# Kernel optimization log

Hardware: AMD Instinct MI355X
Metric: run time of the kernel (lower is better)

## Reference

```python
import jax, jax.numpy as jnp
import numpy as np
import math

EMBED_DIM = 1024
NUM_HEADS = 16
HEAD_DIM = EMBED_DIM // NUM_HEADS
B, S = 2, 2048


def setup_inputs() -> dict:
    key = jax.random.key(0)
    ks = jax.random.split(key, 13)
    sc = 1.0 / math.sqrt(EMBED_DIM)
    inp = {
        "query": jax.random.normal(ks[0], (B, S, EMBED_DIM), jnp.float32),
        "key": jax.random.normal(ks[1], (B, S, EMBED_DIM), jnp.float32),
        "value": jax.random.normal(ks[2], (B, S, EMBED_DIM), jnp.float32),
        "input_patch_mask": jax.random.randint(ks[3], (B, S), 0, 2, jnp.int32),
        "Wq": jax.random.normal(ks[4], (EMBED_DIM, EMBED_DIM), jnp.float32) * sc,
        "bq": jnp.zeros((EMBED_DIM,), jnp.float32),
        "Wk": jax.random.normal(ks[5], (EMBED_DIM, EMBED_DIM), jnp.float32) * sc,
        "bk": jnp.zeros((EMBED_DIM,), jnp.float32),
        "Wv": jax.random.normal(ks[6], (EMBED_DIM, EMBED_DIM), jnp.float32) * sc,
        "bv": jnp.zeros((EMBED_DIM,), jnp.float32),
        "Wo": jax.random.normal(ks[7], (EMBED_DIM, EMBED_DIM), jnp.float32) * sc,
        "bo": jnp.zeros((EMBED_DIM,), jnp.float32),
    }
    return inp


def _masked_softmax(scores, mask):
    # Equivalent to masked_fill(-inf) -> softmax -> nan_to_num(0.0):
    # fully-masked rows produce exactly 0, without generating NaNs.
    neg_inf = jnp.array(-jnp.inf, scores.dtype)
    s = jnp.where(mask, scores, neg_inf)
    m = jnp.max(s, axis=-1, keepdims=True)
    m_safe = jnp.where(jnp.isfinite(m), m, jnp.zeros_like(m))
    e = jnp.where(mask, jnp.exp(s - m_safe), 0.0)
    denom = jnp.sum(e, axis=-1, keepdims=True)
    denom = jnp.where(denom == 0.0, 1.0, denom)
    return e / denom


def reference(query, key, value, input_patch_mask, Wq, bq, Wk, bk, Wv, bv, Wo, bo):
    b, s, d = query.shape
    h, hd = NUM_HEADS, HEAD_DIM
    q = (query @ Wq.T + bq).reshape(b, s, h, hd).transpose(0, 2, 1, 3)  # [b,h,s,hd]
    k = (key @ Wk.T + bk).reshape(b, s, h, hd).transpose(0, 2, 1, 3)
    v = (value @ Wv.T + bv).reshape(b, s, h, hd).transpose(0, 2, 1, 3)
    scores = jnp.einsum("bhqd,bhkd->bhqk", q, k) / math.sqrt(hd)
    # mask[b,i,j] = patch_mask[b,i] * patch_mask[b,j]
    mask = (input_patch_mask[:, :, None] * input_patch_mask[:, None, :]) > 0
    attn = _masked_softmax(scores, mask[:, None, :, :])  # dropout in eval mode = identity
    context = jnp.einsum("bhqk,bhkd->bhqd", attn, v)
    context = context.transpose(0, 2, 1, 3).reshape(b, s, d)
    return context @ Wo.T + bo
```

## Files before the change

kernel.cpp:

```cpp
#include <hip/hip_runtime.h>
#include <cstdint>
#include <cstddef>

#define EMBED 1024
#define NHEAD 16
#define HD    64
#define BATCH 2
#define SEQ   2048
#define MROWS (BATCH*SEQ)
#define QSCALE 0.1803368801111137f

typedef __bf16 bf16;
typedef __bf16 bf16x8 __attribute__((ext_vector_type(8)));
typedef float  f32x4  __attribute__((ext_vector_type(4)));
typedef unsigned int u32;

#if __has_builtin(__builtin_amdgcn_exp2f)
#define EXP2(x) __builtin_amdgcn_exp2f(x)
#else
#define EXP2(x) exp2f(x)
#endif

typedef const u32 __attribute__((address_space(1)))* gp_t;
typedef u32 __attribute__((address_space(3)))* lp_t;

__device__ __forceinline__ void g2l16(const void* g, void* l) {
  __builtin_amdgcn_global_load_lds((gp_t)(uintptr_t)g, (lp_t)(u32)(uintptr_t)l, 16, 0, 0);
}

#define MFMA(a, b, c) __builtin_amdgcn_mfma_f32_16x16x32_bf16((a), (b), (c), 0, 0, 0)

#define SZX8 ((MROWS*EMBED)/8)
#define SZW8 ((EMBED*EMBED)/8)

__global__ void cast_all(const float* __restrict__ q, const float* __restrict__ k,
                         const float* __restrict__ v, const float* __restrict__ wq,
                         const float* __restrict__ wk, const float* __restrict__ wv,
                         const float* __restrict__ wo,
                         bf16* xq, bf16* xk, bf16* xv,
                         bf16* wqb, bf16* wkb, bf16* wvb, bf16* wob) {
  int z = blockIdx.y;
  const float* in; bf16* out;
  switch (z) {
    case 0: in = q;  out = xq;  break;
    case 1: in = k;  out = xk;  break;
    case 2: in = v;  out = xv;  break;
    case 3: in = wq; out = wqb; break;
    case 4: in = wk; out = wkb; break;
    case 5: in = wv; out = wvb; break;
    default: in = wo; out = wob; break;
  }
  int n8 = (z < 3) ? SZX8 : SZW8;
  int i = blockIdx.x * blockDim.x + threadIdx.x;
  if (i >= n8) return;
  const float4* p = (const float4*)in;
  float4 a = p[2*i], b = p[2*i+1];
  union { bf16 h[8]; uint4 u; } r;
  r.h[0] = (bf16)a.x; r.h[1] = (bf16)a.y; r.h[2] = (bf16)a.z; r.h[3] = (bf16)a.w;
  r.h[4] = (bf16)b.x; r.h[5] = (bf16)b.y; r.h[6] = (bf16)b.z; r.h[7] = (bf16)b.w;
  ((uint4*)out)[i] = r.u;
}

#define BM 128
#define BN 128
#define BK 32
#define NKI (EMBED/BK)

__device__ __forceinline__ void gemm_core(
    const bf16* __restrict__ A, const bf16* __restrict__ W,
    bf16* Al, bf16* Bl, f32x4 (&acc)[4][4])
{
  const int tid  = threadIdx.x;
  const int lane = tid & 63, wid = tid >> 6;
  const int quad = lane >> 4, l16 = lane & 15;
  const int wm = wid >> 1, wn = wid & 1;
  const int m0 = blockIdx.y * BM, n0 = blockIdx.x * BN;

  const int R = tid >> 2, Cc = tid & 3;
  const int gcol = (Cc ^ ((R >> 1) & 3)) * 8;
  const bf16* Ag = A + (size_t)(m0 + R) * EMBED + gcol;
  const bf16* Bg = W + (size_t)(n0 + R) * EMBED + gcol;
  bf16* AlW = Al + wid * 512;
  bf16* BlW = Bl + wid * 512;

  g2l16(Ag, AlW);                      g2l16(Ag + (size_t)64*EMBED, AlW + 2048);
  g2l16(Bg, BlW);                      g2l16(Bg + (size_t)64*EMBED, BlW + 2048);
  __syncthreads();

  for (int ki = 0; ki < NKI; ++ki) {
    const int cur = ki & 1;
    if (ki + 1 < NKI) {
      const int nb = cur ^ 1;
      const int k0 = (ki + 1) * BK;
      g2l16(Ag + k0, AlW + nb*4096);
      g2l16(Ag + (size_t)64*EMBED + k0, AlW + nb*4096 + 2048);
      g2l16(Bg + k0, BlW + nb*4096);
      g2l16(Bg + (size_t)64*EMBED + k0, BlW + nb*4096 + 2048);
    }
    const bf16* Ac = Al + cur*4096;
    const bf16* Bc = Bl + cur*4096;
    bf16x8 af[4], bg[4];
#pragma unroll
    for (int i = 0; i < 4; ++i) {
      int ra = wm*64 + i*16 + l16;
      af[i] = *(const bf16x8*)(Ac + ra*32 + ((quad ^ ((ra>>1)&3))*8));
      int rb = wn*64 + i*16 + l16;
      bg[i] = *(const bf16x8*)(Bc + rb*32 + ((quad ^ ((rb>>1)&3))*8));
    }
#pragma unroll
    for (int i = 0; i < 4; ++i)
#pragma unroll
      for (int j = 0; j < 4; ++j)
        acc[i][j] = MFMA(af[i], bg[j], acc[i][j]);
    __syncthreads();
  }
}

__global__ __launch_bounds__(256) void qkv_kernel(
    const bf16* __restrict__ Xq, const bf16* __restrict__ Xk, const bf16* __restrict__ Xv,
    const bf16* __restrict__ Wq, const bf16* __restrict__ Wk, const bf16* __restrict__ Wv,
    const float* __restrict__ bq, const float* __restrict__ bk, const float* __restrict__ bv,
    bf16* __restrict__ Qp, bf16* __restrict__ Kp, bf16* __restrict__ VTg)
{
  __shared__ bf16 Al[2*BM*BK];
  __shared__ bf16 Bl[2*BN*BK];
  const int z = blockIdx.z;
  const bf16* A = z==0 ? Xq : z==1 ? Xk : Xv;
  const bf16* W = z==0 ? Wq : z==1 ? Wk : Wv;
  const float* bias = z==0 ? bq : z==1 ? bk : bv;
  const float scale = (z==0) ? QSCALE : 1.0f;

  f32x4 acc[4][4] = {};
  gemm_core(A, W, Al, Bl, acc);

  const int lane = threadIdx.x & 63, wid = threadIdx.x >> 6;
  const int quad = lane >> 4, l16 = lane & 15;
  const int wm = wid >> 1, wn = wid & 1;
  const int m0 = blockIdx.y * BM, n0 = blockIdx.x * BN;

#pragma unroll
  for (int i = 0; i < 4; ++i) {
#pragma unroll
    for (int j = 0; j < 4; ++j) {
      int col = n0 + wn*64 + j*16 + l16;
      float bv2 = bias[col];
      if (z < 2) {
        bf16* outp = (z == 0) ? Qp : Kp;
#pragma unroll
        for (int r = 0; r < 4; ++r) {
          int row = m0 + wm*64 + i*16 + quad*4 + r;
          outp[(size_t)row*EMBED + col] = (bf16)((acc[i][j][r] + bv2) * scale);
        }
      } else {
        int row0 = m0 + wm*64 + i*16 + quad*4;
        int bb = row0 >> 11, ss0 = row0 & (SEQ-1);
        int hh = col >> 6, dd = col & (HD-1);
        const size_t base = (((size_t)bb*NHEAD + hh)*HD + dd)*SEQ;
#pragma unroll
        for (int r = 0; r < 4; ++r) {
          int s = ss0 + r;
          int tile = s >> 6, loc = s & 63;
          int p = ((loc & 15) << 2) | (loc >> 4);
          VTg[base + tile*64 + p] = (bf16)(acc[i][j][r] + bv2);
        }
      }
    }
  }
}

__global__ __launch_bounds__(256) void oproj_kernel(
    const bf16* __restrict__ Ctx, const bf16* __restrict__ Wo,
    const float* __restrict__ bo, float* __restrict__ out)
{
  __shared__ bf16 Al[2*128*32];
  __shared__ bf16 Bl[2*64*32];
  const int tid  = threadIdx.x;
  const int lane = tid & 63, wid = tid >> 6;
  const int quad = lane >> 4, l16 = lane & 15;
  const int m0 = blockIdx.y * 128, n0 = blockIdx.x * 64;

  const int R = tid >> 2, Cc = tid & 3;
  const int gcol = (Cc ^ ((R >> 1) & 3)) * 8;
  const bf16* Ag = Ctx + (size_t)(m0 + R) * EMBED + gcol;
  const bf16* Bg = Wo  + (size_t)(n0 + R) * EMBED + gcol;
  bf16* AlW = Al + wid * 512;
  bf16* BlW = Bl + wid * 512;

  g2l16(Ag, AlW);  g2l16(Ag + (size_t)64*EMBED, AlW + 2048);
  g2l16(Bg, BlW);
  __syncthreads();

  f32x4 acc[2][4] = {};
  for (int ki = 0; ki < NKI; ++ki) {
    const int cur = ki & 1;
    if (ki + 1 < NKI) {
      const int nb = cur ^ 1;
      const int k0 = (ki + 1) * BK;
      g2l16(Ag + k0, AlW + nb*4096);
      g2l16(Ag + (size_t)64*EMBED + k0, AlW + nb*4096 + 2048);
      g2l16(Bg + k0, BlW + nb*2048);
    }
    const bf16* Ac = Al + cur*4096;
    const bf16* Bc = Bl + cur*2048;
    bf16x8 af[2], bg[4];
#pragma unroll
    for (int u = 0; u < 2; ++u) {
      int ra = wid*32 + u*16 + l16;
      af[u] = *(const bf16x8*)(Ac + ra*32 + ((quad ^ ((ra>>1)&3))*8));
    }
#pragma unroll
    for (int j = 0; j < 4; ++j) {
      int rb = j*16 + l16;
      bg[j] = *(const bf16x8*)(Bc + rb*32 + ((quad ^ ((rb>>1)&3))*8));
    }
#pragma unroll
    for (int u = 0; u < 2; ++u)
#pragma unroll
      for (int j = 0; j < 4; ++j)
        acc[u][j] = MFMA(af[u], bg[j], acc[u][j]);
    __syncthreads();
  }

#pragma unroll
  for (int u = 0; u < 2; ++u)
#pragma unroll
    for (int j = 0; j < 4; ++j) {
      int col = n0 + j*16 + l16;
      float bv = bo[col];
#pragma unroll
      for (int r = 0; r < 4; ++r) {
        int row = m0 + wid*32 + u*16 + quad*4 + r;
        out[(size_t)row*EMBED + col] = (acc[u][j][r] + bv);
      }
    }
}

#define NT  (SEQ/64)
#define PST 72

__global__ __launch_bounds__(512, 4) void attn_kernel(
    const bf16* __restrict__ Qp, const bf16* __restrict__ Kp, const bf16* __restrict__ VT,
    const int* __restrict__ pmask, bf16* __restrict__ Ctx)
{
  __shared__ bf16 Kt[2][64*64];
  __shared__ bf16 Vt[2][64*64];
  __shared__ bf16 Pl[8][16*PST];

  const int qt = blockIdx.x, h = blockIdx.y, b = blockIdx.z;
  const int tid = threadIdx.x, lane = tid & 63, wid = tid >> 6;
  const int quad = lane >> 4, l16 = lane & 15;
  const int qrow0 = qt*128 + wid*16;

  const size_t qoff = (size_t)(b*SEQ + qrow0 + l16)*EMBED + h*HD;
  bf16x8 qf0 = *(const bf16x8*)(Qp + qoff + quad*8);
  bf16x8 qf1 = *(const bf16x8*)(Qp + qoff + 32 + quad*8);

  int qm[4];
#pragma unroll
  for (int r = 0; r < 4; ++r) qm[r] = pmask[b*SEQ + qrow0 + quad*4 + r];

  bf16 onev = (bf16)1.0f;
  bf16x8 ones = {onev, onev, onev, onev, onev, onev, onev, onev};

  const bf16* Kg  = Kp + (size_t)b*SEQ*EMBED + h*HD;
  const bf16* VTg = VT + (size_t)(b*NHEAD + h)*HD*SEQ;

  const int R = tid >> 3;
  const int Cc = tid & 7;
  const int scol = (Cc ^ (R & 7)) * 8;

  f32x4 o[4] = {};
  f32x4 lacc = {};

#define STAGE(kt, buf) do {                                              \
    g2l16(Kg + (size_t)((kt)*64 + R)*EMBED + scol, &Kt[buf][0] + wid*512); \
    g2l16(VTg + (size_t)R*SEQ + (kt)*64 + scol,    &Vt[buf][0] + wid*512); \
  } while (0)

  STAGE(0, 0);
  __syncthreads();

  for (int kt = 0; kt < NT; ++kt) {
    const int cur = kt & 1;
    if (kt + 1 < NT) STAGE(kt + 1, cur ^ 1);
    const bf16* Kc = &Kt[cur][0];
    const bf16* Vc = &Vt[cur][0];

    f32x4 sg[4];
#pragma unroll
    for (int g = 0; g < 4; ++g) {
      int ra = g*16 + l16, sa = ra & 7;
      bf16x8 kfa = *(const bf16x8*)(Kc + ra*64 + ((quad     ^ sa)*8));
      bf16x8 kfb = *(const bf16x8*)(Kc + ra*64 + (((quad+4) ^ sa)*8));
      int km = pmask[b*SEQ + kt*64 + g*16 + l16];
      f32x4 s = {};
      s = MFMA(qf0, kfa, s);
      s = MFMA(qf1, kfb, s);
#pragma unroll
      for (int r = 0; r < 4; ++r) sg[g][r] = km ? EXP2(s[r]) : 0.0f;
    }

#pragma unroll
    for (int r = 0; r < 4; ++r) {
      union { bf16 h[4]; uint2 uu; } pk;
#pragma unroll
      for (int g = 0; g < 4; ++g) pk.h[g] = (bf16)sg[g][r];
      *(uint2*)(&Pl[wid][(quad*4 + r)*PST + l16*4]) = pk.uu;
    }

    bf16x8 pf0 = *(const bf16x8*)(&Pl[wid][l16*PST + quad*8]);
    bf16x8 pf1 = *(const bf16x8*)(&Pl[wid][l16*PST + 32 + quad*8]);
    lacc = MFMA(pf0, ones, lacc);
    lacc = MFMA(pf1, ones, lacc);
#pragma unroll
    for (int t = 0; t < 4; ++t) {
      int rd = t*16 + l16, sd = rd & 7;
      bf16x8 vf0 = *(const bf16x8*)(Vc + rd*64 + ((quad     ^ sd)*8));
      bf16x8 vf1 = *(const bf16x8*)(Vc + rd*64 + (((quad+4) ^ sd)*8));
      o[t] = MFMA(pf0, vf0, o[t]);
      o[t] = MFMA(pf1, vf1, o[t]);
    }
    __syncthreads();
  }

  float inv[4];
#pragma unroll
  for (int r = 0; r < 4; ++r)
    inv[r] = (qm[r] && lacc[r] > 0.f) ? 1.0f / lacc[r] : 0.0f;

#pragma unroll
  for (int t = 0; t < 4; ++t)
#pragma unroll
    for (int r = 0; r < 4; ++r) {
      int row = b*SEQ + qrow0 + quad*4 + r;
      Ctx[(size_t)row*EMBED + h*HD + t*16 + l16] = (bf16)(o[t][r] * inv[r]);
    }
}

extern "C" void kernel_launch(void* const* d_in, const int* in_sizes, int n_in,
                              void* d_out, int out_size, void* d_ws, size_t ws_size,
                              hipStream_t stream)
{
  const float* query = (const float*)d_in[0];
  const float* key   = (const float*)d_in[1];
  const float* value = (const float*)d_in[2];
  const int*   pm    = (const int*)d_in[3];
  const float* Wq = (const float*)d_in[4];
  const float* bq = (const float*)d_in[5];
  const float* Wk = (const float*)d_in[6];
  const float* bk = (const float*)d_in[7];
  const float* Wv = (const float*)d_in[8];
  const float* bv = (const float*)d_in[9];
  const float* Wo = (const float*)d_in[10];
  const float* bo = (const float*)d_in[11];
  float* out = (float*)d_out;

  const size_t SZ_X = (size_t)MROWS * EMBED;
  const size_t SZ_W = (size_t)EMBED * EMBED;

  bf16* p   = (bf16*)d_ws;
  bf16* Xq  = p; p += SZ_X;
  bf16* Xk  = p; p += SZ_X;
  bf16* Xv  = p; p += SZ_X;
  bf16* Wqb = p; p += SZ_W;
  bf16* Wkb = p; p += SZ_W;
  bf16* Wvb = p; p += SZ_W;
  bf16* Wob = p; p += SZ_W;
  bf16* Qp  = p; p += SZ_X;
  bf16* Kp  = p; p += SZ_X;
  bf16* VTg = p; p += SZ_X;
  bf16* Ctx = p; p += SZ_X;

  dim3 gc((unsigned)(SZX8/256), 7);
  cast_all<<<gc, 256, 0, stream>>>(query, key, value, Wq, Wk, Wv, Wo,
                                   Xq, Xk, Xv, Wqb, Wkb, Wvb, Wob);

  dim3 gq(EMBED/BN, MROWS/BM, 3);
  qkv_kernel<<<gq, 256, 0, stream>>>(Xq, Xk, Xv, Wqb, Wkb, Wvb, bq, bk, bv, Qp, Kp, VTg);

  dim3 ga(SEQ/128, NHEAD, BATCH);
  attn_kernel<<<ga, 512, 0, stream>>>(Qp, Kp, VTg, pm, Ctx);

  dim3 gg(EMBED/64, MROWS/128);
  oproj_kernel<<<gg, 256, 0, stream>>>(Ctx, Wob, bo, out);
}
```

Measured before the change: 238.9 us.

## Software-pipeline attention PV with QK and transpose V projection GEMM

The attention loop is restructured so the P·V product for the previous key tile runs after the QK/exp of the current tile. V uses triple-buffered shared memory and P is double-buffered, so the two stages overlap within one barrier per iteration. Separately, the V projection is computed as Wv·Xv^T by swapping operands and block indices, so the transposed VT layout is written with contiguous sequence positions per thread instead of scattered stores. This raises shared memory use per block, which may lower occupancy under the 4-blocks launch bound.

```diff
diff --git a/kernel.cpp b/kernel.cpp
--- a/kernel.cpp
+++ b/kernel.cpp
@@ -68,13 +68,12 @@
 
 __device__ __forceinline__ void gemm_core(
     const bf16* __restrict__ A, const bf16* __restrict__ W,
-    bf16* Al, bf16* Bl, f32x4 (&acc)[4][4])
+    int m0, int n0, bf16* Al, bf16* Bl, f32x4 (&acc)[4][4])
 {
   const int tid  = threadIdx.x;
   const int lane = tid & 63, wid = tid >> 6;
   const int quad = lane >> 4, l16 = lane & 15;
   const int wm = wid >> 1, wn = wid & 1;
-  const int m0 = blockIdx.y * BM, n0 = blockIdx.x * BN;
 
   const int R = tid >> 2, Cc = tid & 3;
   const int gcol = (Cc ^ ((R >> 1) & 3)) * 8;
@@ -125,26 +124,27 @@
   __shared__ bf16 Al[2*BM*BK];
   __shared__ bf16 Bl[2*BN*BK];
   const int z = blockIdx.z;
-  const bf16* A = z==0 ? Xq : z==1 ? Xk : Xv;
-  const bf16* W = z==0 ? Wq : z==1 ? Wk : Wv;
+  const bf16* A = z==0 ? Xq : z==1 ? Xk : Wv;
+  const bf16* W = z==0 ? Wq : z==1 ? Wk : Xv;
   const float* bias = z==0 ? bq : z==1 ? bk : bv;
   const float scale = (z==0) ? QSCALE : 1.0f;
+  const int m0 = (z < 2) ? blockIdx.y * BM : blockIdx.x * BM;
+  const int n0 = (z < 2) ? blockIdx.x * BN : blockIdx.y * BN;
 
   f32x4 acc[4][4] = {};
-  gemm_core(A, W, Al, Bl, acc);
+  gemm_core(A, W, m0, n0, Al, Bl, acc);
 
   const int lane = threadIdx.x & 63, wid = threadIdx.x >> 6;
   const int quad = lane >> 4, l16 = lane & 15;
   const int wm = wid >> 1, wn = wid & 1;
-  const int m0 = blockIdx.y * BM, n0 = blockIdx.x * BN;
 
 #pragma unroll
   for (int i = 0; i < 4; ++i) {
 #pragma unroll
     for (int j = 0; j < 4; ++j) {
       int col = n0 + wn*64 + j*16 + l16;
-      float bv2 = bias[col];
       if (z < 2) {
+        float bv2 = bias[col];
         bf16* outp = (z == 0) ? Qp : Kp;
 #pragma unroll
         for (int r = 0; r < 4; ++r) {
@@ -152,16 +152,16 @@
           outp[(size_t)row*EMBED + col] = (bf16)((acc[i][j][r] + bv2) * scale);
         }
       } else {
-        int row0 = m0 + wm*64 + i*16 + quad*4;
-        int bb = row0 >> 11, ss0 = row0 & (SEQ-1);
-        int hh = col >> 6, dd = col & (HD-1);
-        const size_t base = (((size_t)bb*NHEAD + hh)*HD + dd)*SEQ;
+        int t  = col;
+        int bb = t >> 11, ss = t & (SEQ-1);
+        int tile = ss >> 6;
+        int ppos = l16*4 + (j & 3);
 #pragma unroll
         for (int r = 0; r < 4; ++r) {
-          int s = ss0 + r;
-          int tile = s >> 6, loc = s & 63;
-          int p = ((loc & 15) << 2) | (loc >> 4);
-          VTg[base + tile*64 + p] = (bf16)(acc[i][j][r] + bv2);
+          int e = m0 + wm*64 + i*16 + quad*4 + r;
+          int hh = e >> 6, dd = e & (HD-1);
+          VTg[(((size_t)bb*NHEAD + hh)*HD + dd)*SEQ + tile*64 + ppos]
+              = (bf16)(acc[i][j][r] + bias[e]);
         }
       }
     }
@@ -242,9 +242,9 @@
     const bf16* __restrict__ Qp, const bf16* __restrict__ Kp, const bf16* __restrict__ VT,
     const int* __restrict__ pmask, bf16* __restrict__ Ctx)
 {
-  __shared__ bf16 Kt[2][64*64];
-  __shared__ bf16 Vt[2][64*64];
-  __shared__ bf16 Pl[8][16*PST];
+  __shared__ __align__(16) bf16 Kt[2][64*64];
+  __shared__ __align__(16) bf16 Vt[3][64*64];
+  __shared__ __align__(16) bf16 Pl[2][8][16*PST];
 
   const int qt = blockIdx.x, h = blockIdx.y, b = blockIdx.z;
   const int tid = threadIdx.x, lane = tid & 63, wid = tid >> 6;
@@ -272,20 +272,20 @@
   f32x4 o[4] = {};
   f32x4 lacc = {};
 
-#define STAGE(kt, buf) do {                                              \
-    g2l16(Kg + (size_t)((kt)*64 + R)*EMBED + scol, &Kt[buf][0] + wid*512); \
-    g2l16(VTg + (size_t)R*SEQ + (kt)*64 + scol,    &Vt[buf][0] + wid*512); \
-  } while (0)
-
-  STAGE(0, 0);
+#define STAGE_K(kt, buf) g2l16(Kg + (size_t)((kt)*64 + R)*EMBED + scol, &Kt[buf][0] + wid*512)
+#define STAGE_V(kt, buf) g2l16(VTg + (size_t)R*SEQ + (kt)*64 + scol,    &Vt[buf][0] + wid*512)
+
+  STAGE_K(0, 0);
+  STAGE_V(0, 0);
   __syncthreads();
 
   for (int kt = 0; kt < NT; ++kt) {
-    const int cur = kt & 1;
-    if (kt + 1 < NT) STAGE(kt + 1, cur ^ 1);
-    const bf16* Kc = &Kt[cur][0];
-    const bf16* Vc = &Vt[cur][0];
-
+    if (kt + 1 < NT) {
+      STAGE_K(kt + 1, (kt + 1) & 1);
+      STAGE_V(kt + 1, (kt + 1) % 3);
+    }
+
+    const bf16* Kc = &Kt[kt & 1][0];
     f32x4 sg[4];
 #pragma unroll
     for (int g = 0; g < 4; ++g) {
@@ -300,16 +300,41 @@
       for (int r = 0; r < 4; ++r) sg[g][r] = km ? EXP2(s[r]) : 0.0f;
     }
 
-#pragma unroll
-    for (int r = 0; r < 4; ++r) {
-      union { bf16 h[4]; uint2 uu; } pk;
-#pragma unroll
-      for (int g = 0; g < 4; ++g) pk.h[g] = (bf16)sg[g][r];
-      *(uint2*)(&Pl[wid][(quad*4 + r)*PST + l16*4]) = pk.uu;
-    }
-
-    bf16x8 pf0 = *(const bf16x8*)(&Pl[wid][l16*PST + quad*8]);
-    bf16x8 pf1 = *(const bf16x8*)(&Pl[wid][l16*PST + 32 + quad*8]);
+    if (kt > 0) {
+      const bf16* Vc = &Vt[(kt - 1) % 3][0];
+      bf16* Pw = &Pl[(kt - 1) & 1][wid][0];
+      bf16x8 pf0 = *(const bf16x8*)(Pw + l16*PST + quad*8);
+      bf16x8 pf1 = *(const bf16x8*)(Pw + l16*PST + 32 + quad*8);
+      lacc = MFMA(pf0, ones, lacc);
+      lacc = MFMA(pf1, ones, lacc);
+#pragma unroll
+      for (int t = 0; t < 4; ++t) {
+        int rd = t*16 + l16, sd = rd & 7;
+        bf16x8 vf0 = *(const bf16x8*)(Vc + rd*64 + ((quad     ^ sd)*8));
+        bf16x8 vf1 = *(const bf16x8*)(Vc + rd*64 + (((quad+4) ^ sd)*8));
+        o[t] = MFMA(pf0, vf0, o[t]);
+        o[t] = MFMA(pf1, vf1, o[t]);
+      }
+    }
+
+    {
+      bf16* Pw = &Pl[kt & 1][wid][0];
+#pragma unroll
+      for (int r = 0; r < 4; ++r) {
+        union { bf16 h[4]; uint2 uu; } pk;
+#pragma unroll
+        for (int g = 0; g < 4; ++g) pk.h[g] = (bf16)sg[g][r];
+        *(uint2*)(Pw + (quad*4 + r)*PST + l16*4) = pk.uu;
+      }
+    }
+    __syncthreads();
+  }
+
+  {
+    const bf16* Vc = &Vt[(NT - 1) % 3][0];
+    bf16* Pw = &Pl[(NT - 1) & 1][wid][0];
+    bf16x8 pf0 = *(const bf16x8*)(Pw + l16*PST + quad*8);
+    bf16x8 pf1 = *(const bf16x8*)(Pw + l16*PST + 32 + quad*8);
     lacc = MFMA(pf0, ones, lacc);
     lacc = MFMA(pf1, ones, lacc);
 #pragma unroll
@@ -320,7 +345,6 @@
       o[t] = MFMA(pf0, vf0, o[t]);
       o[t] = MFMA(pf1, vf1, o[t]);
     }
-    __syncthreads();
   }
 
   float inv[4];
```

Measured after the change: 225.5 us. -5.6%, faster.
